# Kernel tuning notes

Hardware: AMD Instinct MI355X
Metric: run time of the kernel (lower is better)

Reference implementation:

```python
import jax, jax.numpy as jnp
import numpy as np

DIAG = 4  # number of distinct power-of-2 diagonal bands; must divide H


def _diag_mask(H, L):
    # head h in group g = h // (H // DIAG) uses tril diagonal offset 2**g - 1.
    # True entries are MASKED (filled with -inf), except the last key column
    # which is always kept (cur_mask[:, -1] = 0 in the torch code).
    group = H // DIAG
    offs = 2 ** (jnp.arange(H) // group) - 1            # [H]
    rows = jnp.arange(L)[:, None]                        # [L,1] query index
    cols = jnp.arange(L)[None, :]                        # [1,L] key index
    mask = (cols <= rows + offs[:, None, None]) & (cols != L - 1)  # [H,L,L]
    return mask


def setup_inputs() -> dict:
    key = jax.random.key(0)
    kq, kk, kv = jax.random.split(key, 3)
    B, L, H, E = 4, 2048, 16, 64
    queries = jax.random.normal(kq, (B, L, H, E), dtype=jnp.float32)
    keys = jax.random.normal(kk, (B, L, H, E), dtype=jnp.float32)
    values = jax.random.normal(kv, (B, L, H, E), dtype=jnp.float32)
    return {"queries": queries, "keys": keys, "values": values}


def reference(queries, keys, values):
    B, L, H, E = queries.shape
    scale = 1.0 / np.sqrt(E).astype(np.float32)
    # [B,H,L,S]
    scores = jnp.einsum('blhe,bshe->bhls', queries, keys)
    mask = _diag_mask(H, L)                              # [H,L,L]
    scores = jnp.where(mask[None], -jnp.inf, scores)
    A = jax.nn.softmax(scale * scores, axis=-1)          # dropout inactive (eval)
    V = jnp.einsum('bhls,bshd->blhd', A, values)
    return V
```

## Files before the change

kernel.cpp:

```cpp
#include <hip/hip_runtime.h>
#include <stdint.h>

using f32x4  = __attribute__((ext_vector_type(4))) float;
using f32x16 = __attribute__((ext_vector_type(16))) float;
using s16x8  = __attribute__((ext_vector_type(8))) short;
using u16x4  = __attribute__((ext_vector_type(4))) unsigned short;
using u32x4  = __attribute__((ext_vector_type(4))) unsigned int;

typedef __attribute__((address_space(3))) unsigned int lds_u32;
typedef __attribute__((address_space(1))) unsigned int glb_u32;

__device__ __forceinline__ unsigned short f2bf(float f){
  union { float f; unsigned u; } x; x.f = f;
  return (unsigned short)((x.u + 0x7FFFu + ((x.u >> 16) & 1u)) >> 16);
}
__device__ __forceinline__ unsigned cvt_pk(float lo, float hi){
  unsigned r;
  asm("v_cvt_pk_bf16_f32 %0, %1, %2" : "=v"(r) : "v"(lo), "v"(hi));
  return r;
}
__device__ __forceinline__ void plswap(unsigned &a, unsigned &b){
  asm volatile("v_permlane32_swap_b32 %0, %1" : "+v"(a), "+v"(b));
}

#if __has_builtin(__builtin_amdgcn_exp2f)
#define EXP2F(x) __builtin_amdgcn_exp2f(x)
#else
#define EXP2F(x) exp2f(x)
#endif

#define MFMA16(A,B,C) __builtin_amdgcn_mfma_f32_16x16x32_bf16((A),(B),(C),0,0,0)
#define MFMA32(A,B,C) __builtin_amdgcn_mfma_f32_32x32x16_bf16((A),(B),(C),0,0,0)

constexpr int   L      = 2048;
constexpr int   H      = 16;
constexpr int   E      = 64;
constexpr int   HE     = 1024;
constexpr float SCALE  = 0.125f;
constexpr float QSCALE = 0.18033688011112042f;

__global__ __launch_bounds__(256)
void prep_kv(const float* __restrict__ Kg, const float* __restrict__ Vg,
             unsigned short* __restrict__ Ko, unsigned short* __restrict__ Vo){
  __shared__ __align__(16) unsigned short t8[4096];
  const int g0 = blockIdx.x;
  const int t  = threadIdx.x;
  if (g0 < 2048){
    const int gid = g0;
    const int jt = gid & 31, bh = gid >> 5;
    const int b = bh >> 4, h = bh & 15;
    const int key6 = t >> 2;
    const int p    = t & 3;
    const int kb = key6 >> 5, k31 = key6 & 31;
    const float* src = Kg + ((size_t)((b*2048 + jt*64 + key6)*16 + h) << 6) + p*16;
    const float4 v0 = *reinterpret_cast<const float4*>(src);
    const float4 v1 = *reinterpret_cast<const float4*>(src + 4);
    const float4 v2 = *reinterpret_cast<const float4*>(src + 8);
    const float4 v3 = *reinterpret_cast<const float4*>(src + 12);
    s16x8 f0, f1;
    f0[0]=(short)f2bf(v0.x); f0[1]=(short)f2bf(v0.y); f0[2]=(short)f2bf(v0.z); f0[3]=(short)f2bf(v0.w);
    f0[4]=(short)f2bf(v1.x); f0[5]=(short)f2bf(v1.y); f0[6]=(short)f2bf(v1.z); f0[7]=(short)f2bf(v1.w);
    f1[0]=(short)f2bf(v2.x); f1[1]=(short)f2bf(v2.y); f1[2]=(short)f2bf(v2.z); f1[3]=(short)f2bf(v2.w);
    f1[4]=(short)f2bf(v3.x); f1[5]=(short)f2bf(v3.y); f1[6]=(short)f2bf(v3.z); f1[7]=(short)f2bf(v3.w);
    const int slot0 = ((kb*4 + p)*2 + 0)*32 + k31;
    *reinterpret_cast<s16x8*>(&t8[slot0*8])      = f0;
    *reinterpret_cast<s16x8*>(&t8[(slot0+32)*8]) = f1;
    __syncthreads();
    unsigned short* dst = Ko + ((size_t)gid << 12) + t*16;
    *reinterpret_cast<s16x8*>(dst)     = *reinterpret_cast<const s16x8*>(&t8[t*16]);
    *reinterpret_cast<s16x8*>(dst + 8) = *reinterpret_cast<const s16x8*>(&t8[t*16 + 8]);
  } else {
    const int gid = g0 - 2048;
    const int jt = gid & 31, bh = gid >> 5;
    const int b = bh >> 4, h = bh & 15;
    const int key6 = t >> 2;
    const int p    = t & 3;
    const int kc = key6 >> 4, h2 = (key6 >> 3) & 1, kr = key6 & 7;
    const float* src = Vg + ((size_t)((b*2048 + jt*64 + key6)*16 + h) << 6) + p*16;
    float vv[16];
    #pragma unroll
    for (int q = 0; q < 4; ++q){
      const float4 v = *reinterpret_cast<const float4*>(src + q*4);
      vv[q*4+0]=v.x; vv[q*4+1]=v.y; vv[q*4+2]=v.z; vv[q*4+3]=v.w;
    }
    #pragma unroll
    for (int j = 0; j < 16; ++j){
      const int e  = p*16 + j;
      const int eb = e >> 5, e31 = e & 31;
      const int slot = ((eb*4 + kc)*2 + h2)*32 + e31;
      t8[slot*8 + kr] = f2bf(vv[j]);
    }
    __syncthreads();
    unsigned short* dst = Vo + ((size_t)gid << 12) + t*16;
    *reinterpret_cast<s16x8*>(dst)     = *reinterpret_cast<const s16x8*>(&t8[t*16]);
    *reinterpret_cast<s16x8*>(dst + 8) = *reinterpret_cast<const s16x8*>(&t8[t*16 + 8]);
  }
}

__global__ __launch_bounds__(256, 4)
void attn6(const float* __restrict__ Qg, const unsigned short* __restrict__ Kbg,
           const unsigned short* __restrict__ Vtg, float* __restrict__ Og)
{
  __shared__ __align__(16) unsigned short Kbuf[2][4096];
  __shared__ __align__(16) unsigned short Vbuf[2][4096];

  const int tid  = threadIdx.x;
  const int wave = tid >> 6;
  const int lane = tid & 63;
  const int c    = lane & 31;
  const int hi   = lane >> 5;

  const int gid = blockIdx.x;
  const int qb  = gid >> 6;
  const int bh  = gid & 63;
  const int b = bh >> 4, h = bh & 15;
  const int off = (1 << (h >> 2)) - 1;

  const int    r0    = 128 * qb;
  const int    qrow0 = r0 + wave * 32;
  const size_t fbase = (size_t)b * L * HE + (size_t)h * 64;
  const size_t tbase = (size_t)bh * 32;

  s16x8 qf[4];
  {
    const float* qp_ = Qg + fbase + (size_t)(qrow0 + c) * HE;
    #pragma unroll
    for (int ec = 0; ec < 4; ++ec){
      const float4 a  = *reinterpret_cast<const float4*>(qp_ + ec*16 + hi*8);
      const float4 b2 = *reinterpret_cast<const float4*>(qp_ + ec*16 + hi*8 + 4);
      s16x8 v;
      v[0]=(short)f2bf(a.x*QSCALE);  v[1]=(short)f2bf(a.y*QSCALE);
      v[2]=(short)f2bf(a.z*QSCALE);  v[3]=(short)f2bf(a.w*QSCALE);
      v[4]=(short)f2bf(b2.x*QSCALE); v[5]=(short)f2bf(b2.y*QSCALE);
      v[6]=(short)f2bf(b2.z*QSCALE); v[7]=(short)f2bf(b2.w*QSCALE);
      qf[ec] = v;
    }
  }

  s16x8 ones;
  #pragma unroll
  for (int j = 0; j < 8; ++j) ones[j] = (short)0x3F80;

  f32x16 acc0, acc1, accl;
  #pragma unroll
  for (int r = 0; r < 16; ++r){ acc0[r]=0.f; acc1[r]=0.f; accl[r]=0.f; }

  const int j0   = 2 * qb;
  const int qlim = qrow0 + c + off;

  auto STAGE = [&](int jt, int nb){
    const unsigned short* gk = Kbg + ((size_t)(tbase + jt) << 12) + (size_t)(wave*128 + lane)*8;
    const unsigned short* gv = Vtg + ((size_t)(tbase + jt) << 12) + (size_t)(wave*128 + lane)*8;
    __builtin_amdgcn_global_load_lds((const glb_u32*)gk,        (lds_u32*)&Kbuf[nb][wave*1024],       16, 0, 0);
    __builtin_amdgcn_global_load_lds((const glb_u32*)(gk+512),  (lds_u32*)&Kbuf[nb][wave*1024 + 512], 16, 0, 0);
    __builtin_amdgcn_global_load_lds((const glb_u32*)gv,        (lds_u32*)&Vbuf[nb][wave*1024],       16, 0, 0);
    __builtin_amdgcn_global_load_lds((const glb_u32*)(gv+512),  (lds_u32*)&Vbuf[nb][wave*1024 + 512], 16, 0, 0);
  };

  auto COMP = [&](int jt, int nb){
    const int s0 = jt * 64;
    if ((jt < 31) && (s0 + 63 <= qrow0 + off)) return;
    const unsigned short* KB = Kbuf[nb];
    const unsigned short* VB = Vbuf[nb];

    f32x16 S0, S1;
    #pragma unroll
    for (int r = 0; r < 16; ++r){ S0[r]=0.f; S1[r]=0.f; }
    __builtin_amdgcn_s_setprio(1);
    #pragma unroll
    for (int ec = 0; ec < 4; ++ec){
      const s16x8 k0 = *reinterpret_cast<const s16x8*>(&KB[(((0*4+ec)*2+hi)*32 + c)*8]);
      const s16x8 k1 = *reinterpret_cast<const s16x8*>(&KB[(((1*4+ec)*2+hi)*32 + c)*8]);
      S0 = MFMA32(k0, qf[ec], S0);
      S1 = MFMA32(k1, qf[ec], S1);
    }
    __builtin_amdgcn_s_setprio(0);

    if ((jt == 31) || (s0 <= qrow0 + 31 + off)){
      #pragma unroll
      for (int r = 0; r < 16; ++r){
        const int kg0 = s0 + (r&3) + 8*(r>>2) + 4*hi;
        const int kg1 = kg0 + 32;
        if (!((kg0 > qlim) || (kg0 == L-1))) S0[r] = -1e30f;
        if (!((kg1 > qlim) || (kg1 == L-1))) S1[r] = -1e30f;
      }
    }

    #pragma unroll
    for (int r = 0; r < 16; ++r){
      S0[r] = EXP2F(S0[r]);
      S1[r] = EXP2F(S1[r]);
    }

    __builtin_amdgcn_s_setprio(1);
    #define PV_STEP(Pv, kh, kcg) { \
      unsigned a0 = cvt_pk(Pv[8*(kh)+0], Pv[8*(kh)+1]); \
      unsigned a1 = cvt_pk(Pv[8*(kh)+2], Pv[8*(kh)+3]); \
      unsigned b0 = cvt_pk(Pv[8*(kh)+4], Pv[8*(kh)+5]); \
      unsigned b1 = cvt_pk(Pv[8*(kh)+6], Pv[8*(kh)+7]); \
      plswap(a0, b0); plswap(a1, b1); \
      u32x4 afu; afu[0]=a0; afu[1]=a1; afu[2]=b0; afu[3]=b1; \
      const s16x8 af = __builtin_bit_cast(s16x8, afu); \
      const s16x8 vf0 = *reinterpret_cast<const s16x8*>(&VB[(((0*4+(kcg))*2+hi)*32 + c)*8]); \
      const s16x8 vf1 = *reinterpret_cast<const s16x8*>(&VB[(((1*4+(kcg))*2+hi)*32 + c)*8]); \
      acc0 = MFMA32(af, vf0, acc0); \
      acc1 = MFMA32(af, vf1, acc1); \
      accl = MFMA32(af, ones, accl); \
    }
    PV_STEP(S0, 0, 0)
    PV_STEP(S0, 1, 1)
    PV_STEP(S1, 0, 2)
    PV_STEP(S1, 1, 3)
    #undef PV_STEP
    __builtin_amdgcn_s_setprio(0);
  };

  #define WAITBAR4 asm volatile("s_waitcnt vmcnt(4)\n\ts_barrier" ::: "memory")
  #define WAITBAR0 asm volatile("s_waitcnt vmcnt(0)\n\ts_barrier" ::: "memory")
  #define BARRIER  asm volatile("s_barrier" ::: "memory")

  STAGE(j0, 0);
  STAGE(j0 + 1, 1);

  for (int jt = j0; jt < 30; jt += 2){
    WAITBAR4;
    COMP(jt, 0);
    BARRIER;
    STAGE(jt + 2, 0);
    WAITBAR4;
    COMP(jt + 1, 1);
    BARRIER;
    STAGE(jt + 3, 1);
  }
  WAITBAR4;
  COMP(30, 0);
  WAITBAR0;
  COMP(31, 1);

  #undef WAITBAR4
  #undef WAITBAR0
  #undef BARRIER

  #pragma unroll
  for (int r = 0; r < 16; ++r){
    const int rowr = (r&3) + 8*(r>>2) + 4*hi;
    const float li = 1.0f / accl[r];
    float* op = Og + fbase + (size_t)(qrow0 + rowr) * HE;
    op[c]      = acc0[r] * li;
    op[32 + c] = acc1[r] * li;
  }
}

__global__ __launch_bounds__(512)
void attn_band(const float* __restrict__ Qg, const float* __restrict__ Kg,
               const float* __restrict__ Vg, float* __restrict__ Og)
{
  __shared__ __align__(16) unsigned short Ks[64*64];
  __shared__ __align__(16) unsigned short Vs[64*64];
  __shared__ __align__(16) unsigned short Ps[8][16*64];
  const int tid  = threadIdx.x;
  const int wave = tid >> 6;
  const int lane = tid & 63;
  const int lo16 = lane & 15;
  const int hi4  = lane >> 4;
  const int gid = blockIdx.x;
  const int qb  = gid & 15;
  const int bh  = gid >> 4;
  const int b   = bh >> 4;
  const int h   = bh & 15;
  const int off = (1 << (h >> 2)) - 1;
  const int    r0   = qb * 128;
  const size_t base = (size_t)b * L * HE + (size_t)h * 64;
  const int qrow0 = r0 + wave * 16;
  s16x8 qf[2];
  {
    const float* qp = Qg + base + (size_t)(qrow0 + lo16) * HE;
    #pragma unroll
    for (int ec = 0; ec < 2; ++ec){
      const int e0 = ec*32 + hi4*8;
      s16x8 v;
      #pragma unroll
      for (int j = 0; j < 8; ++j) v[j] = (short)f2bf(qp[e0 + j]);
      qf[ec] = v;
    }
  }
  f32x4 acc[4];
  #pragma unroll
  for (int et = 0; et < 4; ++et) acc[et] = f32x4{0.f,0.f,0.f,0.f};
  float m_run[4], l_run[4];
  #pragma unroll
  for (int i = 0; i < 4; ++i){ m_run[i] = -1e30f; l_run[i] = 0.f; }
  const int j0 = (r0 + off + 1) >> 6;
  for (int jt = j0; jt < 32; ++jt){
    const int s0 = jt * 64;
    __syncthreads();
    {
      const int f4    = tid & 15;
      const int rbase = tid >> 4;
      #pragma unroll
      for (int p = 0; p < 2; ++p){
        const int row = p*32 + rbase;
        const float4 vv = *reinterpret_cast<const float4*>(
            Kg + base + (size_t)(s0 + row) * HE + f4*4);
        u16x4 w; w[0]=f2bf(vv.x); w[1]=f2bf(vv.y); w[2]=f2bf(vv.z); w[3]=f2bf(vv.w);
        const int idx = row*64 + ((f4*4) ^ ((row & 7) << 3));
        *reinterpret_cast<u16x4*>(&Ks[idx]) = w;
      }
    }
    {
      const int kb = tid >> 5;
      const int e0 = (tid & 31) * 2;
      float2 cc[4];
      #pragma unroll
      for (int j = 0; j < 4; ++j)
        cc[j] = *reinterpret_cast<const float2*>(
            Vg + base + (size_t)(s0 + 4*kb + j) * HE + e0);
      #pragma unroll
      for (int i = 0; i < 2; ++i){
        const int e = e0 + i;
        u16x4 w;
        w[0] = f2bf(i ? cc[0].y : cc[0].x);
        w[1] = f2bf(i ? cc[1].y : cc[1].x);
        w[2] = f2bf(i ? cc[2].y : cc[2].x);
        w[3] = f2bf(i ? cc[3].y : cc[3].x);
        const int idx = e*64 + ((kb*4) ^ ((e & 7) << 3));
        *reinterpret_cast<u16x4*>(&Vs[idx]) = w;
      }
    }
    __syncthreads();
    if (jt < 31 && s0 + 63 <= qrow0 + off) continue;
    f32x4 S[4];
    #pragma unroll
    for (int kt = 0; kt < 4; ++kt){
      const int key = kt*16 + lo16;
      f32x4 z = {0.f,0.f,0.f,0.f};
      #pragma unroll
      for (int ec = 0; ec < 2; ++ec){
        const int e = ec*32 + hi4*8;
        const s16x8 kf = *reinterpret_cast<const s16x8*>(
            &Ks[key*64 + (e ^ ((key & 7) << 3))]);
        z = MFMA16(qf[ec], kf, z);
      }
      S[kt] = z;
    }
    #pragma unroll
    for (int kt = 0; kt < 4; ++kt){
      const int kg = s0 + kt*16 + lo16;
      #pragma unroll
      for (int i = 0; i < 4; ++i){
        const int qg2 = qrow0 + hi4*4 + i;
        const bool ok = (kg > qg2 + off) || (kg == L-1);
        S[kt][i] = ok ? S[kt][i]*SCALE : -1e30f;
      }
    }
    #pragma unroll
    for (int i = 0; i < 4; ++i){
      float t = fmaxf(fmaxf(S[0][i],S[1][i]), fmaxf(S[2][i],S[3][i]));
      t = fmaxf(t, __shfl_xor(t,1));
      t = fmaxf(t, __shfl_xor(t,2));
      t = fmaxf(t, __shfl_xor(t,4));
      t = fmaxf(t, __shfl_xor(t,8));
      const float mn = fmaxf(m_run[i], t);
      const float rs = __expf(m_run[i] - mn);
      m_run[i]  = mn;
      l_run[i] *= rs;
      acc[0][i] *= rs; acc[1][i] *= rs; acc[2][i] *= rs; acc[3][i] *= rs;
    }
    unsigned short* pwv = Ps[wave];
    float rsum[4] = {0.f,0.f,0.f,0.f};
    #pragma unroll
    for (int kt = 0; kt < 4; ++kt){
      #pragma unroll
      for (int i = 0; i < 4; ++i){
        const float p = __expf(S[kt][i] - m_run[i]);
        rsum[i] += p;
        const int qr  = hi4*4 + i;
        const int col = kt*16 + lo16;
        pwv[qr*64 + (col ^ ((qr & 7) << 3))] = f2bf(p);
      }
    }
    #pragma unroll
    for (int i = 0; i < 4; ++i){
      float t = rsum[i];
      t += __shfl_xor(t,1); t += __shfl_xor(t,2);
      t += __shfl_xor(t,4); t += __shfl_xor(t,8);
      l_run[i] += t;
    }
    #pragma unroll
    for (int kc = 0; kc < 2; ++kc){
      const int kk = kc*32 + hi4*8;
      const s16x8 pf = *reinterpret_cast<const s16x8*>(
          &pwv[lo16*64 + (kk ^ ((lo16 & 7) << 3))]);
      #pragma unroll
      for (int et = 0; et < 4; ++et){
        const int e = et*16 + lo16;
        const s16x8 vf = *reinterpret_cast<const s16x8*>(
            &Vs[e*64 + (kk ^ ((e & 7) << 3))]);
        acc[et] = MFMA16(pf, vf, acc[et]);
      }
    }
  }
  #pragma unroll
  for (int i = 0; i < 4; ++i){
    const float inv = 1.0f / l_run[i];
    const int   qg2 = qrow0 + hi4*4 + i;
    float* op = Og + base + (size_t)qg2 * HE;
    #pragma unroll
    for (int et = 0; et < 4; ++et)
      op[et*16 + lo16] = acc[et][i] * inv;
  }
}

extern "C" void kernel_launch(void* const* d_in, const int* in_sizes, int n_in,
                              void* d_out, int out_size, void* d_ws, size_t ws_size,
                              hipStream_t stream) {
  const float* Q = (const float*)d_in[0];
  const float* K = (const float*)d_in[1];
  const float* V = (const float*)d_in[2];
  float* O = (float*)d_out;

  const size_t kb_bytes = (size_t)64 * 32 * 4096 * 2;
  const size_t need     = kb_bytes * 2;
  if (ws_size >= need) {
    unsigned short* Kb = (unsigned short*)d_ws;
    unsigned short* Vt = (unsigned short*)((char*)d_ws + kb_bytes);
    prep_kv<<<dim3(4096), dim3(256), 0, stream>>>(K, V, Kb, Vt);
    attn6  <<<dim3(1024), dim3(256), 0, stream>>>(Q, Kb, Vt, O);
  } else {
    attn_band<<<dim3(1024), dim3(512), 0, stream>>>(Q, K, V, O);
  }
}
```

Before: 72.58 us.

## Process two query sub-tiles per wave with triple-buffered K/V and balanced block order

Each wave now handles 64 query rows (two 32-row sub-tiles) instead of 32, so every K/V tile loaded into LDS feeds twice as many MFMAs. The grid is halved to 512 blocks, and query blocks are paired so light and heavy blocks are interleaved for load balance. The K/V staging moves from double to triple buffering with one barrier per tile, so the next load is issued before compute. In exchange register pressure roughly doubles (launch bounds drop to 2 blocks per SM), fewer waves are resident, and the STAGE address mapping is changed.

```diff
diff --git a/kernel.cpp b/kernel.cpp
--- a/kernel.cpp
+++ b/kernel.cpp
@@ -97,12 +97,12 @@
   }
 }
 
-__global__ __launch_bounds__(256, 4)
-void attn6(const float* __restrict__ Qg, const unsigned short* __restrict__ Kbg,
+__global__ __launch_bounds__(256, 2)
+void attn7(const float* __restrict__ Qg, const unsigned short* __restrict__ Kbg,
            const unsigned short* __restrict__ Vtg, float* __restrict__ Og)
 {
-  __shared__ __align__(16) unsigned short Kbuf[2][4096];
-  __shared__ __align__(16) unsigned short Vbuf[2][4096];
+  __shared__ __align__(16) unsigned short Kbuf[3][4096];
+  __shared__ __align__(16) unsigned short Vbuf[3][4096];
 
   const int tid  = threadIdx.x;
   const int wave = tid >> 6;
@@ -111,29 +111,37 @@
   const int hi   = lane >> 5;
 
   const int gid = blockIdx.x;
-  const int qb  = gid >> 6;
+  const int u   = gid >> 6;
   const int bh  = gid & 63;
+  const int qb  = (u < 4) ? u : 11 - u;
   const int b = bh >> 4, h = bh & 15;
   const int off = (1 << (h >> 2)) - 1;
 
-  const int    r0    = 128 * qb;
-  const int    qrow0 = r0 + wave * 32;
+  const int    r0    = 256 * qb;
+  const int    qrow0 = r0 + wave * 64;
   const size_t fbase = (size_t)b * L * HE + (size_t)h * 64;
   const size_t tbase = (size_t)bh * 32;
 
-  s16x8 qf[4];
+  s16x8 qfa[4], qfb[4];
   {
-    const float* qp_ = Qg + fbase + (size_t)(qrow0 + c) * HE;
+    const float* qpa = Qg + fbase + (size_t)(qrow0 + c) * HE;
+    const float* qpb = Qg + fbase + (size_t)(qrow0 + 32 + c) * HE;
     #pragma unroll
     for (int ec = 0; ec < 4; ++ec){
-      const float4 a  = *reinterpret_cast<const float4*>(qp_ + ec*16 + hi*8);
-      const float4 b2 = *reinterpret_cast<const float4*>(qp_ + ec*16 + hi*8 + 4);
-      s16x8 v;
-      v[0]=(short)f2bf(a.x*QSCALE);  v[1]=(short)f2bf(a.y*QSCALE);
-      v[2]=(short)f2bf(a.z*QSCALE);  v[3]=(short)f2bf(a.w*QSCALE);
-      v[4]=(short)f2bf(b2.x*QSCALE); v[5]=(short)f2bf(b2.y*QSCALE);
-      v[6]=(short)f2bf(b2.z*QSCALE); v[7]=(short)f2bf(b2.w*QSCALE);
-      qf[ec] = v;
+      float4 a0 = *reinterpret_cast<const float4*>(qpa + ec*16 + hi*8);
+      float4 a1 = *reinterpret_cast<const float4*>(qpa + ec*16 + hi*8 + 4);
+      float4 b0 = *reinterpret_cast<const float4*>(qpb + ec*16 + hi*8);
+      float4 b1 = *reinterpret_cast<const float4*>(qpb + ec*16 + hi*8 + 4);
+      s16x8 va, vb;
+      va[0]=(short)f2bf(a0.x*QSCALE); va[1]=(short)f2bf(a0.y*QSCALE);
+      va[2]=(short)f2bf(a0.z*QSCALE); va[3]=(short)f2bf(a0.w*QSCALE);
+      va[4]=(short)f2bf(a1.x*QSCALE); va[5]=(short)f2bf(a1.y*QSCALE);
+      va[6]=(short)f2bf(a1.z*QSCALE); va[7]=(short)f2bf(a1.w*QSCALE);
+      vb[0]=(short)f2bf(b0.x*QSCALE); vb[1]=(short)f2bf(b0.y*QSCALE);
+      vb[2]=(short)f2bf(b0.z*QSCALE); vb[3]=(short)f2bf(b0.w*QSCALE);
+      vb[4]=(short)f2bf(b1.x*QSCALE); vb[5]=(short)f2bf(b1.y*QSCALE);
+      vb[6]=(short)f2bf(b1.z*QSCALE); vb[7]=(short)f2bf(b1.w*QSCALE);
+      qfa[ec] = va; qfb[ec] = vb;
     }
   }
 
@@ -141,16 +149,20 @@
   #pragma unroll
   for (int j = 0; j < 8; ++j) ones[j] = (short)0x3F80;
 
-  f32x16 acc0, acc1, accl;
-  #pragma unroll
-  for (int r = 0; r < 16; ++r){ acc0[r]=0.f; acc1[r]=0.f; accl[r]=0.f; }
-
-  const int j0   = 2 * qb;
-  const int qlim = qrow0 + c + off;
+  f32x16 acca0, acca1, accla, accb0, accb1, acclb;
+  #pragma unroll
+  for (int r = 0; r < 16; ++r){
+    acca0[r]=0.f; acca1[r]=0.f; accla[r]=0.f;
+    accb0[r]=0.f; accb1[r]=0.f; acclb[r]=0.f;
+  }
+
+  const int j0     = 4 * qb;
+  const int qlim_a = qrow0 + c + off;
+  const int qlim_b = qlim_a + 32;
 
   auto STAGE = [&](int jt, int nb){
-    const unsigned short* gk = Kbg + ((size_t)(tbase + jt) << 12) + (size_t)(wave*128 + lane)*8;
-    const unsigned short* gv = Vtg + ((size_t)(tbase + jt) << 12) + (size_t)(wave*128 + lane)*8;
+    const unsigned short* gk = Kbg + ((size_t)(tbase + jt) << 12) + (size_t)(wave*1024 + lane*8);
+    const unsigned short* gv = Vtg + ((size_t)(tbase + jt) << 12) + (size_t)(wave*1024 + lane*8);
     __builtin_amdgcn_global_load_lds((const glb_u32*)gk,        (lds_u32*)&Kbuf[nb][wave*1024],       16, 0, 0);
     __builtin_amdgcn_global_load_lds((const glb_u32*)(gk+512),  (lds_u32*)&Kbuf[nb][wave*1024 + 512], 16, 0, 0);
     __builtin_amdgcn_global_load_lds((const glb_u32*)gv,        (lds_u32*)&Vbuf[nb][wave*1024],       16, 0, 0);
@@ -160,94 +172,107 @@
   auto COMP = [&](int jt, int nb){
     const int s0 = jt * 64;
     if ((jt < 31) && (s0 + 63 <= qrow0 + off)) return;
-    const unsigned short* KB = Kbuf[nb];
-    const unsigned short* VB = Vbuf[nb];
-
-    f32x16 S0, S1;
-    #pragma unroll
-    for (int r = 0; r < 16; ++r){ S0[r]=0.f; S1[r]=0.f; }
+    const unsigned short* KB = &Kbuf[nb][0];
+    const unsigned short* VB = &Vbuf[nb][0];
+
+    f32x16 Sa0, Sa1, Sb0, Sb1;
+    #pragma unroll
+    for (int r = 0; r < 16; ++r){ Sa0[r]=0.f; Sa1[r]=0.f; Sb0[r]=0.f; Sb1[r]=0.f; }
     __builtin_amdgcn_s_setprio(1);
     #pragma unroll
     for (int ec = 0; ec < 4; ++ec){
       const s16x8 k0 = *reinterpret_cast<const s16x8*>(&KB[(((0*4+ec)*2+hi)*32 + c)*8]);
       const s16x8 k1 = *reinterpret_cast<const s16x8*>(&KB[(((1*4+ec)*2+hi)*32 + c)*8]);
-      S0 = MFMA32(k0, qf[ec], S0);
-      S1 = MFMA32(k1, qf[ec], S1);
+      Sa0 = MFMA32(k0, qfa[ec], Sa0);
+      Sb0 = MFMA32(k0, qfb[ec], Sb0);
+      Sa1 = MFMA32(k1, qfa[ec], Sa1);
+      Sb1 = MFMA32(k1, qfb[ec], Sb1);
     }
     __builtin_amdgcn_s_setprio(0);
 
-    if ((jt == 31) || (s0 <= qrow0 + 31 + off)){
+    if ((jt == 31) || (s0 <= qrow0 + 63 + off)){
       #pragma unroll
       for (int r = 0; r < 16; ++r){
         const int kg0 = s0 + (r&3) + 8*(r>>2) + 4*hi;
         const int kg1 = kg0 + 32;
-        if (!((kg0 > qlim) || (kg0 == L-1))) S0[r] = -1e30f;
-        if (!((kg1 > qlim) || (kg1 == L-1))) S1[r] = -1e30f;
+        if (!((kg0 > qlim_a) || (kg0 == L-1))) Sa0[r] = -1e30f;
+        if (!((kg1 > qlim_a) || (kg1 == L-1))) Sa1[r] = -1e30f;
+        if (!((kg0 > qlim_b) || (kg0 == L-1))) Sb0[r] = -1e30f;
+        if (!((kg1 > qlim_b) || (kg1 == L-1))) Sb1[r] = -1e30f;
       }
     }
 
     #pragma unroll
     for (int r = 0; r < 16; ++r){
-      S0[r] = EXP2F(S0[r]);
-      S1[r] = EXP2F(S1[r]);
+      Sa0[r] = EXP2F(Sa0[r]);
+      Sa1[r] = EXP2F(Sa1[r]);
+      Sb0[r] = EXP2F(Sb0[r]);
+      Sb1[r] = EXP2F(Sb1[r]);
     }
 
     __builtin_amdgcn_s_setprio(1);
-    #define PV_STEP(Pv, kh, kcg) { \
-      unsigned a0 = cvt_pk(Pv[8*(kh)+0], Pv[8*(kh)+1]); \
-      unsigned a1 = cvt_pk(Pv[8*(kh)+2], Pv[8*(kh)+3]); \
-      unsigned b0 = cvt_pk(Pv[8*(kh)+4], Pv[8*(kh)+5]); \
-      unsigned b1 = cvt_pk(Pv[8*(kh)+6], Pv[8*(kh)+7]); \
-      plswap(a0, b0); plswap(a1, b1); \
-      u32x4 afu; afu[0]=a0; afu[1]=a1; afu[2]=b0; afu[3]=b1; \
-      const s16x8 af = __builtin_bit_cast(s16x8, afu); \
+    #define PV_STEP(PvA, PvB, kh, kcg) { \
+      unsigned aa0 = cvt_pk(PvA[8*(kh)+0], PvA[8*(kh)+1]); \
+      unsigned aa1 = cvt_pk(PvA[8*(kh)+2], PvA[8*(kh)+3]); \
+      unsigned ah0 = cvt_pk(PvA[8*(kh)+4], PvA[8*(kh)+5]); \
+      unsigned ah1 = cvt_pk(PvA[8*(kh)+6], PvA[8*(kh)+7]); \
+      plswap(aa0, ah0); plswap(aa1, ah1); \
+      u32x4 afu; afu[0]=aa0; afu[1]=aa1; afu[2]=ah0; afu[3]=ah1; \
+      const s16x8 afa = __builtin_bit_cast(s16x8, afu); \
+      unsigned ba0 = cvt_pk(PvB[8*(kh)+0], PvB[8*(kh)+1]); \
+      unsigned ba1 = cvt_pk(PvB[8*(kh)+2], PvB[8*(kh)+3]); \
+      unsigned bh0 = cvt_pk(PvB[8*(kh)+4], PvB[8*(kh)+5]); \
+      unsigned bh1 = cvt_pk(PvB[8*(kh)+6], PvB[8*(kh)+7]); \
+      plswap(ba0, bh0); plswap(ba1, bh1); \
+      u32x4 bfu; bfu[0]=ba0; bfu[1]=ba1; bfu[2]=bh0; bfu[3]=bh1; \
+      const s16x8 afb = __builtin_bit_cast(s16x8, bfu); \
       const s16x8 vf0 = *reinterpret_cast<const s16x8*>(&VB[(((0*4+(kcg))*2+hi)*32 + c)*8]); \
       const s16x8 vf1 = *reinterpret_cast<const s16x8*>(&VB[(((1*4+(kcg))*2+hi)*32 + c)*8]); \
-      acc0 = MFMA32(af, vf0, acc0); \
-      acc1 = MFMA32(af, vf1, acc1); \
-      accl = MFMA32(af, ones, accl); \
-    }
-    PV_STEP(S0, 0, 0)
-    PV_STEP(S0, 1, 1)
-    PV_STEP(S1, 0, 2)
-    PV_STEP(S1, 1, 3)
+      acca0 = MFMA32(afa, vf0, acca0); \
+      accb0 = MFMA32(afb, vf0, accb0); \
+      acca1 = MFMA32(afa, vf1, acca1); \
+      accb1 = MFMA32(afb, vf1, accb1); \
+      accla = MFMA32(afa, ones, accla); \
+      acclb = MFMA32(afb, ones, acclb); \
+    }
+    PV_STEP(Sa0, Sb0, 0, 0)
+    PV_STEP(Sa0, Sb0, 1, 1)
+    PV_STEP(Sa1, Sb1, 0, 2)
+    PV_STEP(Sa1, Sb1, 1, 3)
     #undef PV_STEP
     __builtin_amdgcn_s_setprio(0);
   };
 
-  #define WAITBAR4 asm volatile("s_waitcnt vmcnt(4)\n\ts_barrier" ::: "memory")
-  #define WAITBAR0 asm volatile("s_waitcnt vmcnt(0)\n\ts_barrier" ::: "memory")
-  #define BARRIER  asm volatile("s_barrier" ::: "memory")
-
   STAGE(j0, 0);
   STAGE(j0 + 1, 1);
-
-  for (int jt = j0; jt < 30; jt += 2){
-    WAITBAR4;
-    COMP(jt, 0);
-    BARRIER;
-    STAGE(jt + 2, 0);
-    WAITBAR4;
-    COMP(jt + 1, 1);
-    BARRIER;
-    STAGE(jt + 3, 1);
-  }
-  WAITBAR4;
-  COMP(30, 0);
-  WAITBAR0;
-  COMP(31, 1);
-
-  #undef WAITBAR4
-  #undef WAITBAR0
-  #undef BARRIER
+  int nb = 0, sb = 2;
+  for (int jt = j0; jt < 30; ++jt){
+    asm volatile("s_waitcnt vmcnt(4)" ::: "memory");
+    __builtin_amdgcn_s_barrier();
+    STAGE(jt + 2, sb);
+    COMP(jt, nb);
+    nb = (nb == 2) ? 0 : nb + 1;
+    sb = (sb == 2) ? 0 : sb + 1;
+  }
+  asm volatile("s_waitcnt vmcnt(4)" ::: "memory");
+  __builtin_amdgcn_s_barrier();
+  COMP(30, nb);
+  nb = (nb == 2) ? 0 : nb + 1;
+  asm volatile("s_waitcnt vmcnt(0)" ::: "memory");
+  __builtin_amdgcn_s_barrier();
+  COMP(31, nb);
 
   #pragma unroll
   for (int r = 0; r < 16; ++r){
     const int rowr = (r&3) + 8*(r>>2) + 4*hi;
-    const float li = 1.0f / accl[r];
-    float* op = Og + fbase + (size_t)(qrow0 + rowr) * HE;
-    op[c]      = acc0[r] * li;
-    op[32 + c] = acc1[r] * li;
+    const float lia = 1.0f / accla[r];
+    const float lib = 1.0f / acclb[r];
+    float* opa = Og + fbase + (size_t)(qrow0 + rowr) * HE;
+    float* opb = Og + fbase + (size_t)(qrow0 + 32 + rowr) * HE;
+    opa[c]      = acca0[r] * lia;
+    opa[32 + c] = acca1[r] * lia;
+    opb[c]      = accb0[r] * lib;
+    opb[32 + c] = accb1[r] * lib;
   }
 }
 
@@ -425,7 +450,7 @@
     unsigned short* Kb = (unsigned short*)d_ws;
     unsigned short* Vt = (unsigned short*)((char*)d_ws + kb_bytes);
     prep_kv<<<dim3(4096), dim3(256), 0, stream>>>(K, V, Kb, Vt);
-    attn6  <<<dim3(1024), dim3(256), 0, stream>>>(Q, Kb, Vt, O);
+    attn7  <<<dim3(512),  dim3(256), 0, stream>>>(Q, Kb, Vt, O);
   } else {
     attn_band<<<dim3(1024), dim3(512), 0, stream>>>(Q, K, V, O);
   }
```

Result: slower. 77.29 us (+6.5%).

## Replace LDS-staged multi-wave attention with single-wave register-prefetch kernel

Applied to the files above, without the earlier changes.

The attention kernel now runs one 64-lane wave per block over 32 query rows, launched as 4096 blocks. K and V fragments load directly from global memory into registers with a two-deep software prefetch, replacing the LDS double-buffering and its block barriers. Each wave's starting key tile is computed from its own rows, so only unmasked tiles are visited. This removes barrier stalls and LDS traffic, but waves no longer share staged tiles, so L2 traffic rises and register pressure grows from the prefetched fragments.

```diff
diff --git a/kernel.cpp b/kernel.cpp
--- a/kernel.cpp
+++ b/kernel.cpp
@@ -6,9 +6,6 @@
 using s16x8  = __attribute__((ext_vector_type(8))) short;
 using u16x4  = __attribute__((ext_vector_type(4))) unsigned short;
 using u32x4  = __attribute__((ext_vector_type(4))) unsigned int;
-
-typedef __attribute__((address_space(3))) unsigned int lds_u32;
-typedef __attribute__((address_space(1))) unsigned int glb_u32;
 
 __device__ __forceinline__ unsigned short f2bf(float f){
   union { float f; unsigned u; } x; x.f = f;
@@ -97,27 +94,24 @@
   }
 }
 
-__global__ __launch_bounds__(256, 4)
-void attn6(const float* __restrict__ Qg, const unsigned short* __restrict__ Kbg,
+struct KF { s16x8 a[8]; };
+struct VF { s16x8 a[8]; };
+
+__global__ __launch_bounds__(64, 2)
+void attn9(const float* __restrict__ Qg, const unsigned short* __restrict__ Kbg,
            const unsigned short* __restrict__ Vtg, float* __restrict__ Og)
 {
-  __shared__ __align__(16) unsigned short Kbuf[2][4096];
-  __shared__ __align__(16) unsigned short Vbuf[2][4096];
-
-  const int tid  = threadIdx.x;
-  const int wave = tid >> 6;
-  const int lane = tid & 63;
+  const int lane = threadIdx.x & 63;
   const int c    = lane & 31;
   const int hi   = lane >> 5;
 
   const int gid = blockIdx.x;
-  const int qb  = gid >> 6;
+  const int qc  = gid >> 6;
   const int bh  = gid & 63;
   const int b = bh >> 4, h = bh & 15;
   const int off = (1 << (h >> 2)) - 1;
 
-  const int    r0    = 128 * qb;
-  const int    qrow0 = r0 + wave * 32;
+  const int    qrow0 = 32 * qc;
   const size_t fbase = (size_t)b * L * HE + (size_t)h * 64;
   const size_t tbase = (size_t)bh * 32;
 
@@ -145,37 +139,33 @@
   #pragma unroll
   for (int r = 0; r < 16; ++r){ acc0[r]=0.f; acc1[r]=0.f; accl[r]=0.f; }
 
-  const int j0   = 2 * qb;
+  const int j0   = (qrow0 + off + 1) >> 6;
   const int qlim = qrow0 + c + off;
 
-  auto STAGE = [&](int jt, int nb){
-    const unsigned short* gk = Kbg + ((size_t)(tbase + jt) << 12) + (size_t)(wave*128 + lane)*8;
-    const unsigned short* gv = Vtg + ((size_t)(tbase + jt) << 12) + (size_t)(wave*128 + lane)*8;
-    __builtin_amdgcn_global_load_lds((const glb_u32*)gk,        (lds_u32*)&Kbuf[nb][wave*1024],       16, 0, 0);
-    __builtin_amdgcn_global_load_lds((const glb_u32*)(gk+512),  (lds_u32*)&Kbuf[nb][wave*1024 + 512], 16, 0, 0);
-    __builtin_amdgcn_global_load_lds((const glb_u32*)gv,        (lds_u32*)&Vbuf[nb][wave*1024],       16, 0, 0);
-    __builtin_amdgcn_global_load_lds((const glb_u32*)(gv+512),  (lds_u32*)&Vbuf[nb][wave*1024 + 512], 16, 0, 0);
+  auto loadK = [&](int jt, KF& f){
+    const unsigned short* g = Kbg + ((size_t)(tbase + jt) << 12);
+    #pragma unroll
+    for (int x = 0; x < 8; ++x)
+      f.a[x] = *reinterpret_cast<const s16x8*>(&g[((x*2 + hi)*32 + c)*8]);
   };
-
-  auto COMP = [&](int jt, int nb){
-    const int s0 = jt * 64;
-    if ((jt < 31) && (s0 + 63 <= qrow0 + off)) return;
-    const unsigned short* KB = Kbuf[nb];
-    const unsigned short* VB = Vbuf[nb];
-
-    f32x16 S0, S1;
+  auto loadV = [&](int jt, VF& f){
+    const unsigned short* g = Vtg + ((size_t)(tbase + jt) << 12);
+    #pragma unroll
+    for (int x = 0; x < 8; ++x)
+      f.a[x] = *reinterpret_cast<const s16x8*>(&g[((x*2 + hi)*32 + c)*8]);
+  };
+
+  auto QKEXP = [&](int jt, const KF& kf, f32x16& S0, f32x16& S1){
     #pragma unroll
     for (int r = 0; r < 16; ++r){ S0[r]=0.f; S1[r]=0.f; }
     __builtin_amdgcn_s_setprio(1);
     #pragma unroll
     for (int ec = 0; ec < 4; ++ec){
-      const s16x8 k0 = *reinterpret_cast<const s16x8*>(&KB[(((0*4+ec)*2+hi)*32 + c)*8]);
-      const s16x8 k1 = *reinterpret_cast<const s16x8*>(&KB[(((1*4+ec)*2+hi)*32 + c)*8]);
-      S0 = MFMA32(k0, qf[ec], S0);
-      S1 = MFMA32(k1, qf[ec], S1);
+      S0 = MFMA32(kf.a[ec],     qf[ec], S0);
+      S1 = MFMA32(kf.a[4 + ec], qf[ec], S1);
     }
     __builtin_amdgcn_s_setprio(0);
-
+    const int s0 = jt * 64;
     if ((jt == 31) || (s0 <= qrow0 + 31 + off)){
       #pragma unroll
       for (int r = 0; r < 16; ++r){
@@ -185,13 +175,14 @@
         if (!((kg1 > qlim) || (kg1 == L-1))) S1[r] = -1e30f;
       }
     }
-
     #pragma unroll
     for (int r = 0; r < 16; ++r){
       S0[r] = EXP2F(S0[r]);
       S1[r] = EXP2F(S1[r]);
     }
-
+  };
+
+  auto PV = [&](const f32x16& S0, const f32x16& S1, const VF& vf){
     __builtin_amdgcn_s_setprio(1);
     #define PV_STEP(Pv, kh, kcg) { \
       unsigned a0 = cvt_pk(Pv[8*(kh)+0], Pv[8*(kh)+1]); \
@@ -201,10 +192,8 @@
       plswap(a0, b0); plswap(a1, b1); \
       u32x4 afu; afu[0]=a0; afu[1]=a1; afu[2]=b0; afu[3]=b1; \
       const s16x8 af = __builtin_bit_cast(s16x8, afu); \
-      const s16x8 vf0 = *reinterpret_cast<const s16x8*>(&VB[(((0*4+(kcg))*2+hi)*32 + c)*8]); \
-      const s16x8 vf1 = *reinterpret_cast<const s16x8*>(&VB[(((1*4+(kcg))*2+hi)*32 + c)*8]); \
-      acc0 = MFMA32(af, vf0, acc0); \
-      acc1 = MFMA32(af, vf1, acc1); \
+      acc0 = MFMA32(af, vf.a[(kcg)],     acc0); \
+      acc1 = MFMA32(af, vf.a[4 + (kcg)], acc1); \
       accl = MFMA32(af, ones, accl); \
     }
     PV_STEP(S0, 0, 0)
@@ -215,31 +204,26 @@
     __builtin_amdgcn_s_setprio(0);
   };
 
-  #define WAITBAR4 asm volatile("s_waitcnt vmcnt(4)\n\ts_barrier" ::: "memory")
-  #define WAITBAR0 asm volatile("s_waitcnt vmcnt(0)\n\ts_barrier" ::: "memory")
-  #define BARRIER  asm volatile("s_barrier" ::: "memory")
-
-  STAGE(j0, 0);
-  STAGE(j0 + 1, 1);
-
-  for (int jt = j0; jt < 30; jt += 2){
-    WAITBAR4;
-    COMP(jt, 0);
-    BARRIER;
-    STAGE(jt + 2, 0);
-    WAITBAR4;
-    COMP(jt + 1, 1);
-    BARRIER;
-    STAGE(jt + 3, 1);
-  }
-  WAITBAR4;
-  COMP(30, 0);
-  WAITBAR0;
-  COMP(31, 1);
-
-  #undef WAITBAR4
-  #undef WAITBAR0
-  #undef BARRIER
+  KF kA, kB; VF vA, vB;
+  f32x16 S0, S1;
+
+  loadK(j0, kA);
+  loadV(j0, vA);
+
+  for (int jt = j0; jt < 31; jt += 2){
+    loadK(jt + 1, kB);
+    QKEXP(jt, kA, S0, S1);
+    loadV(jt + 1, vB);
+    PV(S0, S1, vA);
+    if (jt + 2 < 32) loadK(jt + 2, kA);
+    QKEXP(jt + 1, kB, S0, S1);
+    if (jt + 2 < 32) loadV(jt + 2, vA);
+    PV(S0, S1, vB);
+  }
+  if (j0 & 1){
+    QKEXP(31, kA, S0, S1);
+    PV(S0, S1, vA);
+  }
 
   #pragma unroll
   for (int r = 0; r < 16; ++r){
@@ -425,7 +409,7 @@
     unsigned short* Kb = (unsigned short*)d_ws;
     unsigned short* Vt = (unsigned short*)((char*)d_ws + kb_bytes);
     prep_kv<<<dim3(4096), dim3(256), 0, stream>>>(K, V, Kb, Vt);
-    attn6  <<<dim3(1024), dim3(256), 0, stream>>>(Q, Kb, Vt, O);
+    attn9  <<<dim3(4096), dim3(64),  0, stream>>>(Q, Kb, Vt, O);
   } else {
     attn_band<<<dim3(1024), dim3(512), 0, stream>>>(Q, K, V, O);
   }
```

Result: slower. 77.43 us (+6.7%).

## Load V directly to registers, compute row sums with VALU, reorder query blocks

Applied to the files above, without the earlier changes.

Restructures the attention kernel so V tiles are loaded straight from global memory into registers, one tile ahead, rather than staged through LDS. Only K stays in a double-buffered LDS, with a single barrier per tile. The ones-vector MFMA used for the softmax denominator is replaced by VALU sums plus a cross-lane shuffle. Query blocks are assigned in a zig-zag order to balance causal work across blocks. This cuts LDS traffic and MFMA work but raises register pressure and exposes global V latency.

```diff
diff --git a/kernel.cpp b/kernel.cpp
--- a/kernel.cpp
+++ b/kernel.cpp
@@ -97,12 +97,13 @@
   }
 }
 
+struct VF { s16x8 a[8]; };
+
 __global__ __launch_bounds__(256, 4)
-void attn6(const float* __restrict__ Qg, const unsigned short* __restrict__ Kbg,
-           const unsigned short* __restrict__ Vtg, float* __restrict__ Og)
+void attn10(const float* __restrict__ Qg, const unsigned short* __restrict__ Kbg,
+            const unsigned short* __restrict__ Vtg, float* __restrict__ Og)
 {
   __shared__ __align__(16) unsigned short Kbuf[2][4096];
-  __shared__ __align__(16) unsigned short Vbuf[2][4096];
 
   const int tid  = threadIdx.x;
   const int wave = tid >> 6;
@@ -111,8 +112,10 @@
   const int hi   = lane >> 5;
 
   const int gid = blockIdx.x;
-  const int qb  = gid >> 6;
+  const int u   = gid >> 6;
   const int bh  = gid & 63;
+  const int k   = u >> 2, u0 = u & 3;
+  const int qb  = (k & 1) ? (15 - 2*u0 - (k >> 1)) : (2*u0 + (k >> 1));
   const int b = bh >> 4, h = bh & 15;
   const int off = (1 << (h >> 2)) - 1;
 
@@ -137,114 +140,118 @@
     }
   }
 
-  s16x8 ones;
+  f32x16 acc0, acc1;
   #pragma unroll
-  for (int j = 0; j < 8; ++j) ones[j] = (short)0x3F80;
-
-  f32x16 acc0, acc1, accl;
-  #pragma unroll
-  for (int r = 0; r < 16; ++r){ acc0[r]=0.f; acc1[r]=0.f; accl[r]=0.f; }
+  for (int r = 0; r < 16; ++r){ acc0[r]=0.f; acc1[r]=0.f; }
+  float l_run = 0.f;
 
   const int j0   = 2 * qb;
   const int qlim = qrow0 + c + off;
 
-  auto STAGE = [&](int jt, int nb){
-    const unsigned short* gk = Kbg + ((size_t)(tbase + jt) << 12) + (size_t)(wave*128 + lane)*8;
-    const unsigned short* gv = Vtg + ((size_t)(tbase + jt) << 12) + (size_t)(wave*128 + lane)*8;
-    __builtin_amdgcn_global_load_lds((const glb_u32*)gk,        (lds_u32*)&Kbuf[nb][wave*1024],       16, 0, 0);
-    __builtin_amdgcn_global_load_lds((const glb_u32*)(gk+512),  (lds_u32*)&Kbuf[nb][wave*1024 + 512], 16, 0, 0);
-    __builtin_amdgcn_global_load_lds((const glb_u32*)gv,        (lds_u32*)&Vbuf[nb][wave*1024],       16, 0, 0);
-    __builtin_amdgcn_global_load_lds((const glb_u32*)(gv+512),  (lds_u32*)&Vbuf[nb][wave*1024 + 512], 16, 0, 0);
+  auto STAGE_K = [&](int jt, int nb){
+    const unsigned short* gk = Kbg + ((size_t)(tbase + jt) << 12) + (size_t)(wave*1024 + lane*8);
+    __builtin_amdgcn_global_load_lds((const glb_u32*)gk,
+        (lds_u32*)&Kbuf[nb][wave*1024], 16, 0, 0);
+    __builtin_amdgcn_global_load_lds((const glb_u32*)(gk + 512),
+        (lds_u32*)&Kbuf[nb][wave*1024 + 512], 16, 0, 0);
   };
-
-  auto COMP = [&](int jt, int nb){
+  auto loadV = [&](int jt, VF& f){
+    const unsigned short* g = Vtg + ((size_t)(tbase + jt) << 12);
+    #pragma unroll
+    for (int x = 0; x < 8; ++x)
+      f.a[x] = *reinterpret_cast<const s16x8*>(&g[((x*2 + hi)*32 + c)*8]);
+  };
+
+  VF vA;
+  f32x16 S0, S1;
+
+  asm volatile("s_waitcnt vmcnt(0)" ::: "memory");
+  STAGE_K(j0, j0 & 1);
+  asm volatile("" ::: "memory");
+  loadV(j0, vA);
+
+  for (int jt = j0; jt < 32; ++jt){
+    asm volatile("s_waitcnt vmcnt(8)" ::: "memory");
+    __builtin_amdgcn_s_barrier();
+    if (jt < 31){
+      STAGE_K(jt + 1, (jt + 1) & 1);
+      asm volatile("" ::: "memory");
+    }
+
     const int s0 = jt * 64;
-    if ((jt < 31) && (s0 + 63 <= qrow0 + off)) return;
-    const unsigned short* KB = Kbuf[nb];
-    const unsigned short* VB = Vbuf[nb];
-
-    f32x16 S0, S1;
-    #pragma unroll
-    for (int r = 0; r < 16; ++r){ S0[r]=0.f; S1[r]=0.f; }
-    __builtin_amdgcn_s_setprio(1);
-    #pragma unroll
-    for (int ec = 0; ec < 4; ++ec){
-      const s16x8 k0 = *reinterpret_cast<const s16x8*>(&KB[(((0*4+ec)*2+hi)*32 + c)*8]);
-      const s16x8 k1 = *reinterpret_cast<const s16x8*>(&KB[(((1*4+ec)*2+hi)*32 + c)*8]);
-      S0 = MFMA32(k0, qf[ec], S0);
-      S1 = MFMA32(k1, qf[ec], S1);
-    }
-    __builtin_amdgcn_s_setprio(0);
-
-    if ((jt == 31) || (s0 <= qrow0 + 31 + off)){
+    const bool live = !((jt < 31) && (s0 + 63 <= qrow0 + off));
+    if (live){
+      const unsigned short* KB = &Kbuf[jt & 1][0];
+
+      #pragma unroll
+      for (int r = 0; r < 16; ++r){ S0[r]=0.f; S1[r]=0.f; }
+      __builtin_amdgcn_s_setprio(1);
+      #pragma unroll
+      for (int ec = 0; ec < 4; ++ec){
+        const s16x8 k0 = *reinterpret_cast<const s16x8*>(&KB[(((0*4+ec)*2+hi)*32 + c)*8]);
+        const s16x8 k1 = *reinterpret_cast<const s16x8*>(&KB[(((1*4+ec)*2+hi)*32 + c)*8]);
+        S0 = MFMA32(k0, qf[ec], S0);
+        S1 = MFMA32(k1, qf[ec], S1);
+      }
+      __builtin_amdgcn_s_setprio(0);
+
+      if ((jt == 31) || (s0 <= qrow0 + 31 + off)){
+        #pragma unroll
+        for (int r = 0; r < 16; ++r){
+          const int kg0 = s0 + (r&3) + 8*(r>>2) + 4*hi;
+          const int kg1 = kg0 + 32;
+          if (!((kg0 > qlim) || (kg0 == L-1))) S0[r] = -1e30f;
+          if (!((kg1 > qlim) || (kg1 == L-1))) S1[r] = -1e30f;
+        }
+      }
+
       #pragma unroll
       for (int r = 0; r < 16; ++r){
-        const int kg0 = s0 + (r&3) + 8*(r>>2) + 4*hi;
-        const int kg1 = kg0 + 32;
-        if (!((kg0 > qlim) || (kg0 == L-1))) S0[r] = -1e30f;
-        if (!((kg1 > qlim) || (kg1 == L-1))) S1[r] = -1e30f;
-      }
-    }
-
-    #pragma unroll
-    for (int r = 0; r < 16; ++r){
-      S0[r] = EXP2F(S0[r]);
-      S1[r] = EXP2F(S1[r]);
-    }
-
-    __builtin_amdgcn_s_setprio(1);
-    #define PV_STEP(Pv, kh, kcg) { \
-      unsigned a0 = cvt_pk(Pv[8*(kh)+0], Pv[8*(kh)+1]); \
-      unsigned a1 = cvt_pk(Pv[8*(kh)+2], Pv[8*(kh)+3]); \
-      unsigned b0 = cvt_pk(Pv[8*(kh)+4], Pv[8*(kh)+5]); \
-      unsigned b1 = cvt_pk(Pv[8*(kh)+6], Pv[8*(kh)+7]); \
-      plswap(a0, b0); plswap(a1, b1); \
-      u32x4 afu; afu[0]=a0; afu[1]=a1; afu[2]=b0; afu[3]=b1; \
-      const s16x8 af = __builtin_bit_cast(s16x8, afu); \
-      const s16x8 vf0 = *reinterpret_cast<const s16x8*>(&VB[(((0*4+(kcg))*2+hi)*32 + c)*8]); \
-      const s16x8 vf1 = *reinterpret_cast<const s16x8*>(&VB[(((1*4+(kcg))*2+hi)*32 + c)*8]); \
-      acc0 = MFMA32(af, vf0, acc0); \
-      acc1 = MFMA32(af, vf1, acc1); \
-      accl = MFMA32(af, ones, accl); \
-    }
-    PV_STEP(S0, 0, 0)
-    PV_STEP(S0, 1, 1)
-    PV_STEP(S1, 0, 2)
-    PV_STEP(S1, 1, 3)
-    #undef PV_STEP
-    __builtin_amdgcn_s_setprio(0);
-  };
-
-  #define WAITBAR4 asm volatile("s_waitcnt vmcnt(4)\n\ts_barrier" ::: "memory")
-  #define WAITBAR0 asm volatile("s_waitcnt vmcnt(0)\n\ts_barrier" ::: "memory")
-  #define BARRIER  asm volatile("s_barrier" ::: "memory")
-
-  STAGE(j0, 0);
-  STAGE(j0 + 1, 1);
-
-  for (int jt = j0; jt < 30; jt += 2){
-    WAITBAR4;
-    COMP(jt, 0);
-    BARRIER;
-    STAGE(jt + 2, 0);
-    WAITBAR4;
-    COMP(jt + 1, 1);
-    BARRIER;
-    STAGE(jt + 3, 1);
-  }
-  WAITBAR4;
-  COMP(30, 0);
-  WAITBAR0;
-  COMP(31, 1);
-
-  #undef WAITBAR4
-  #undef WAITBAR0
-  #undef BARRIER
-
+        S0[r] = EXP2F(S0[r]);
+        S1[r] = EXP2F(S1[r]);
+      }
+      {
+        float p0=0.f, p1=0.f, p2=0.f, p3=0.f;
+        #pragma unroll
+        for (int r = 0; r < 16; r += 4){
+          p0 += S0[r] + S1[r];
+          p1 += S0[r+1] + S1[r+1];
+          p2 += S0[r+2] + S1[r+2];
+          p3 += S0[r+3] + S1[r+3];
+        }
+        float ps = (p0 + p1) + (p2 + p3);
+        ps += __shfl_xor(ps, 32);
+        l_run += ps;
+      }
+
+      __builtin_amdgcn_s_setprio(1);
+      #define PV_STEP(Pv, kh, kcg) { \
+        unsigned a0 = cvt_pk(Pv[8*(kh)+0], Pv[8*(kh)+1]); \
+        unsigned a1 = cvt_pk(Pv[8*(kh)+2], Pv[8*(kh)+3]); \
+        unsigned b0 = cvt_pk(Pv[8*(kh)+4], Pv[8*(kh)+5]); \
+        unsigned b1 = cvt_pk(Pv[8*(kh)+6], Pv[8*(kh)+7]); \
+        plswap(a0, b0); plswap(a1, b1); \
+        u32x4 afu; afu[0]=a0; afu[1]=a1; afu[2]=b0; afu[3]=b1; \
+        const s16x8 af = __builtin_bit_cast(s16x8, afu); \
+        acc0 = MFMA32(af, vA.a[(kcg)],     acc0); \
+        acc1 = MFMA32(af, vA.a[4 + (kcg)], acc1); \
+      }
+      PV_STEP(S0, 0, 0)
+      PV_STEP(S0, 1, 1)
+      PV_STEP(S1, 0, 2)
+      PV_STEP(S1, 1, 3)
+      #undef PV_STEP
+      __builtin_amdgcn_s_setprio(0);
+    }
+
+    if (jt < 31) loadV(jt + 1, vA);
+  }
+
+  const float inv = 1.0f / l_run;
   #pragma unroll
   for (int r = 0; r < 16; ++r){
     const int rowr = (r&3) + 8*(r>>2) + 4*hi;
-    const float li = 1.0f / accl[r];
+    const float li = __shfl(inv, rowr);
     float* op = Og + fbase + (size_t)(qrow0 + rowr) * HE;
     op[c]      = acc0[r] * li;
     op[32 + c] = acc1[r] * li;
@@ -425,7 +432,7 @@
     unsigned short* Kb = (unsigned short*)d_ws;
     unsigned short* Vt = (unsigned short*)((char*)d_ws + kb_bytes);
     prep_kv<<<dim3(4096), dim3(256), 0, stream>>>(K, V, Kb, Vt);
-    attn6  <<<dim3(1024), dim3(256), 0, stream>>>(Q, Kb, Vt, O);
+    attn10 <<<dim3(1024), dim3(256), 0, stream>>>(Q, Kb, Vt, O);
   } else {
     attn_band<<<dim3(1024), dim3(512), 0, stream>>>(Q, K, V, O);
   }
```

Result: slower. 98.68 us (+36.0%).
